# Performance work log

Measured on AMD Instinct MI355X. Metric: run time of the kernel, lower is better.

## Reference

```python
import jax, jax.numpy as jnp
import numpy as np

B, N, C_IN, HID, K, DEG = 8192, 64, 128, 128, 5, 8


def setup_inputs() -> dict:
    key = jax.random.key(0)
    ks = jax.random.split(key, 8)
    total = B * N
    E = B * N * DEG
    x = jax.random.normal(ks[0], (total, C_IN), dtype=jnp.float32)
    batch = jnp.repeat(jnp.arange(B, dtype=jnp.int64), N)
    g = jnp.repeat(jnp.arange(B, dtype=jnp.int64), N * DEG)
    src = g * N + jax.random.randint(ks[1], (E,), 0, N).astype(jnp.int64)
    dst = g * N + jax.random.randint(ks[2], (E,), 0, N).astype(jnp.int64)
    edge_index = jnp.stack([src, dst])  # [2, E]
    s = 0.05
    return {
        "x": x,
        "edge_index": edge_index,
        "batch": batch,
        "W_pool": jax.random.normal(ks[3], (C_IN, K), dtype=jnp.float32) * s,
        "b_pool": jnp.zeros((K,), jnp.float32),
        "W1": jax.random.normal(ks[4], (C_IN, HID), dtype=jnp.float32) * s,
        "b1": jnp.zeros((HID,), jnp.float32),
        "W2": jax.random.normal(ks[5], (HID, HID), dtype=jnp.float32) * s,
        "b2": jnp.zeros((HID,), jnp.float32),
        "W_lin": jax.random.normal(ks[6], (HID, 1), dtype=jnp.float32) * s,
        "b_lin": jnp.zeros((1,), jnp.float32),
        "num_graphs": B,
        "max_nodes": N,
    }


def dense_gcn(x, adj, W, b, mask=None):
    # PyG DenseGCNConv with add_loop=True: diagonal set to 1 on a copy
    n = adj.shape[1]
    idx = jnp.arange(n)
    adj_l = adj.at[:, idx, idx].set(1.0)
    out = x @ W  # [B, n, out]
    d = jnp.clip(adj_l.sum(-1), 1.0) ** -0.5  # [B, n]
    adj_n = d[:, :, None] * adj_l * d[:, None, :]
    out = jnp.einsum('bnm,bmc->bnc', adj_n, out) + b
    if mask is not None:
        out = out * mask[..., None]
    return out


def reference(x, edge_index, batch, W_pool, b_pool, W1, b1, W2, b2, W_lin, b_lin,
              num_graphs, max_nodes):
    total = x.shape[0]
    # to_dense_batch: position of each node within its graph (batch is sorted)
    first_idx = jax.ops.segment_min(jnp.arange(total), batch, num_segments=num_graphs)
    pos = jnp.arange(total) - first_idx[batch]
    x_dense = jnp.zeros((num_graphs, max_nodes, x.shape[1]), x.dtype).at[batch, pos].set(x)
    mask = jnp.zeros((num_graphs, max_nodes), x.dtype).at[batch, pos].set(1.0)
    # to_dense_adj
    src, dst = edge_index[0], edge_index[1]
    adj = jnp.zeros((num_graphs, max_nodes, max_nodes), x.dtype)
    adj = adj.at[batch[src], pos[src], pos[dst]].add(1.0)

    s = dense_gcn(x_dense, adj, W_pool, b_pool, mask)       # [B, N, K]
    x_l1 = dense_gcn(x_dense, adj, W1, b1, mask)            # [B, N, H]

    # dense_diff_pool (losses are discarded by the original forward)
    s = jax.nn.softmax(s, axis=-1) * mask[..., None]
    xm = x_l1 * mask[..., None]
    x_p1 = jnp.einsum('bnk,bnc->bkc', s, xm)                # [B, K, H]
    adj_p1 = jnp.einsum('bnk,bnm,bml->bkl', s, adj, s)      # [B, K, K]

    x_l2 = dense_gcn(x_p1, adj_p1, W2, b2)                  # [B, K, H]
    pooled = x_l2.sum(axis=1)                               # global_add_pool -> [B, H]
    return pooled @ W_lin + b_lin                           # [B, 1]
```

## Files before the change

### kernel.cpp

```cpp
#include <hip/hip_runtime.h>
#include <hip/hip_bf16.h>

#define NN 64
#define CI 128
#define HD 128
#define KC 5
#define SXS 136
#define AJW 17

#define WS_Z   9216
#define WS_B1Z 9344
#define WS_B2W 9345

typedef float v4f __attribute__((ext_vector_type(4)));
typedef __bf16 v8bf __attribute__((ext_vector_type(8)));
typedef unsigned short us8 __attribute__((ext_vector_type(8)));

__device__ __forceinline__ float us2f(unsigned short u) {
    union { unsigned i; float f; } v; v.i = ((unsigned)u) << 16; return v.f;
}
__device__ __forceinline__ unsigned short f2us(float f) {
    __hip_bfloat16 h = __float2bfloat16(f);
    return *reinterpret_cast<unsigned short*>(&h);
}

extern "C" __global__ void zprep(const float* __restrict__ W1,
                                 const float* __restrict__ Wp,
                                 const float* __restrict__ W2,
                                 const float* __restrict__ Wl,
                                 const float* __restrict__ b1,
                                 const float* __restrict__ b2,
                                 float* __restrict__ ws)
{
    const int b = blockIdx.x, t = threadIdx.x;
    if (b < 36) {
        const int ct = b >> 2, ks = b & 3;
        const int q = t >> 4, m16 = t & 15;
        const int k0 = ks * 32 + q * 8;
        us8 pk;
        #pragma unroll
        for (int j = 0; j < 8; ++j) {
            const int k = k0 + j;
            float v;
            if (ct < 8)      v = W1[k * HD + ct * 16 + m16];
            else             v = (m16 < KC) ? Wp[k * KC + m16] : 0.f;
            pk[j] = f2us(v);
        }
        reinterpret_cast<us8*>(ws)[b * 64 + t] = pk;
    } else if (b == 36) {
        float a0 = 0.f, a1 = 0.f;
        for (int c = 0; c < HD; ++c) {
            const float wl = Wl[c];
            a0 += W2[t * HD + c] * wl;
            a1 += W2[(t + 64) * HD + c] * wl;
        }
        ws[WS_Z + t] = a0;
        ws[WS_Z + 64 + t] = a1;
        float p1 = b1[t] * a0 + b1[t + 64] * a1;
        float p2 = b2[t] * Wl[t] + b2[t + 64] * Wl[t + 64];
        #pragma unroll
        for (int off = 32; off; off >>= 1) {
            p1 += __shfl_down(p1, off, 64);
            p2 += __shfl_down(p2, off, 64);
        }
        if (t == 0) { ws[WS_B1Z] = p1; ws[WS_B2W] = p2; }
    }
}

extern "C" __global__ __launch_bounds__(256, 5)
void diffpool_main(const float* __restrict__ x,
                   const int* __restrict__ ei,
                   const float* __restrict__ bp,
                   const float* __restrict__ bl,
                   const float* __restrict__ ws,
                   float* __restrict__ out,
                   int E, int epg)
{
    __shared__ __attribute__((aligned(16))) unsigned short sx[NN][SXS];
    __shared__ unsigned int sadjb[NN][AJW];
    __shared__ float sSm[NN][KC];
    __shared__ float spart[4][NN * KC];
    __shared__ float sz [HD];
    __shared__ float sqp[2][NN];
    __shared__ float sd [NN];
    __shared__ float sw_[NN];
    __shared__ unsigned int srdeg[NN];
    __shared__ float spp[4][25];
    __shared__ float sadjp[25];
    __shared__ float sd2[KC];
    __shared__ float scoef[KC + 1];

    const int t = threadIdx.x;
    const int g = blockIdx.x;
    const int lane = t & 63;
    const int wv = t >> 6;
    const int n = lane;
    const int h = wv;

    int e0s = -1, e0d = 0, e1s = -1, e1d = 0;
    const int base = g * epg;
    if (t < epg)       { e0s = ei[base + t] & 63;        e0d = ei[E + base + t] & 63; }
    if (t + 256 < epg) { e1s = ei[base + t + 256] & 63;  e1d = ei[E + base + t + 256] & 63; }

    {
        unsigned int* ap = &sadjb[0][0];
        for (int i = t; i < NN * AJW; i += 256) ap[i] = 0u;
        if (t < NN) srdeg[t] = 0u;
        const float* xg = x + (size_t)g * (NN * CI);
        #pragma unroll
        for (int i = 0; i < 4; ++i) {
            const int idx = t + 256 * i;
            const int row = idx >> 4, ch = idx & 15;
            const float4 v0 = *reinterpret_cast<const float4*>(xg + row * CI + ch * 8);
            const float4 v1 = *reinterpret_cast<const float4*>(xg + row * CI + ch * 8 + 4);
            us8 pk;
            pk[0] = f2us(v0.x); pk[1] = f2us(v0.y); pk[2] = f2us(v0.z); pk[3] = f2us(v0.w);
            pk[4] = f2us(v1.x); pk[5] = f2us(v1.y); pk[6] = f2us(v1.z); pk[7] = f2us(v1.w);
            *reinterpret_cast<us8*>(&sx[row][ch * 8]) = pk;
        }
        if (t < 32)
            reinterpret_cast<float4*>(sz)[t] = reinterpret_cast<const float4*>(ws + WS_Z)[t];
    }
    __syncthreads();

    {
        if (e0s >= 0) {
            atomicAdd(&sadjb[e0s][e0d >> 2], 1u << ((e0d & 3) * 8));
            atomicAdd(&srdeg[e0s], 1u);
        }
        if (e1s >= 0) {
            atomicAdd(&sadjb[e1s][e1d >> 2], 1u << ((e1d & 3) * 8));
            atomicAdd(&srdeg[e1s], 1u);
        }
        for (int j = t + 512; j < epg; j += 256) {
            const int sn = ei[base + j] & 63;
            const int dn = ei[E + base + j] & 63;
            atomicAdd(&sadjb[sn][dn >> 2], 1u << ((dn & 3) * 8));
            atomicAdd(&srdeg[sn], 1u);
        }
    }
    __syncthreads();

    {
        const int m16 = lane & 15;
        const int q = lane >> 4;
        const int arow = wv * 16 + m16;
        v8bf afrag[4];
        #pragma unroll
        for (int ks = 0; ks < 4; ++ks)
            afrag[ks] = *reinterpret_cast<const v8bf*>(&sx[arow][ks * 32 + q * 8]);
        const v8bf* wpk = reinterpret_cast<const v8bf*>(ws);
        #pragma unroll
        for (int ct = 0; ct < 9; ++ct) {
            v4f acc = {0.f, 0.f, 0.f, 0.f};
            #pragma unroll
            for (int ks = 0; ks < 4; ++ks) {
                const v8bf bfrag = wpk[(ct * 4 + ks) * 64 + lane];
                acc = __builtin_amdgcn_mfma_f32_16x16x32_bf16(afrag[ks], bfrag, acc, 0, 0, 0);
            }
            if (ct < 8) {
                #pragma unroll
                for (int r = 0; r < 4; ++r)
                    sx[wv * 16 + q * 4 + r][ct * 16 + m16] = f2us(acc[r]);
            } else if (m16 < KC) {
                #pragma unroll
                for (int r = 0; r < 4; ++r)
                    sSm[wv * 16 + q * 4 + r][m16] = acc[r];
            }
        }
    }
    if (t < NN) {
        const unsigned self = (sadjb[t][t >> 2] >> ((t & 3) * 8)) & 255u;
        sd[t] = rsqrtf((float)(srdeg[t] + 1u - self));
    }
    __syncthreads();

    {
        float a0 = 0.f, a1 = 0.f, a2 = 0.f, a3 = 0.f, a4 = 0.f;
        #pragma unroll
        for (int i = 0; i < 4; ++i) {
            const unsigned w = sadjb[n][h * 4 + i];
            #pragma unroll
            for (int b = 0; b < 4; ++b) {
                const int m = h * 16 + i * 4 + b;
                const float al = (m == n) ? 1.f : (float)((w >> (b * 8)) & 255u);
                const float f = al * sd[m];
                a0 += f * sSm[m][0]; a1 += f * sSm[m][1]; a2 += f * sSm[m][2];
                a3 += f * sSm[m][3]; a4 += f * sSm[m][4];
            }
        }
        float* pp = &spart[h][n * KC];
        pp[0] = a0; pp[1] = a1; pp[2] = a2; pp[3] = a3; pp[4] = a4;
    }
    __syncthreads();

    if (wv == 0) {
        float a0 = spart[0][n*KC+0] + spart[1][n*KC+0] + spart[2][n*KC+0] + spart[3][n*KC+0];
        float a1 = spart[0][n*KC+1] + spart[1][n*KC+1] + spart[2][n*KC+1] + spart[3][n*KC+1];
        float a2 = spart[0][n*KC+2] + spart[1][n*KC+2] + spart[2][n*KC+2] + spart[3][n*KC+2];
        float a3 = spart[0][n*KC+3] + spart[1][n*KC+3] + spart[2][n*KC+3] + spart[3][n*KC+3];
        float a4 = spart[0][n*KC+4] + spart[1][n*KC+4] + spart[2][n*KC+4] + spart[3][n*KC+4];
        const float dn = sd[n];
        a0 = a0 * dn + bp[0]; a1 = a1 * dn + bp[1]; a2 = a2 * dn + bp[2];
        a3 = a3 * dn + bp[3]; a4 = a4 * dn + bp[4];
        const float mx = fmaxf(fmaxf(fmaxf(a0, a1), fmaxf(a2, a3)), a4);
        a0 = expf(a0 - mx); a1 = expf(a1 - mx); a2 = expf(a2 - mx);
        a3 = expf(a3 - mx); a4 = expf(a4 - mx);
        const float inv = 1.f / (a0 + a1 + a2 + a3 + a4);
        sSm[n][0] = a0 * inv; sSm[n][1] = a1 * inv; sSm[n][2] = a2 * inv;
        sSm[n][3] = a3 * inv; sSm[n][4] = a4 * inv;
    } else if (wv <= 2) {
        const int p = wv - 1, m = lane;
        float a = 0.f;
        #pragma unroll
        for (int cc = 0; cc < 8; ++cc) {
            const int c = (cc + (m >> 3)) & 7;
            const us8 hh = *reinterpret_cast<const us8*>(&sx[m][p * 64 + c * 8]);
            #pragma unroll
            for (int j = 0; j < 8; ++j) a += us2f(hh[j]) * sz[p * 64 + c * 8 + j];
        }
        sqp[p][m] = a;
    }
    __syncthreads();

    {
        float u0 = 0.f, u1 = 0.f, u2 = 0.f, u3 = 0.f, u4 = 0.f;
        #pragma unroll
        for (int i = 0; i < 4; ++i) {
            const unsigned w = sadjb[n][h * 4 + i];
            #pragma unroll
            for (int b = 0; b < 4; ++b) {
                const int m = h * 16 + i * 4 + b;
                const float c = (float)((w >> (b * 8)) & 255u);
                u0 += c * sSm[m][0]; u1 += c * sSm[m][1]; u2 += c * sSm[m][2];
                u3 += c * sSm[m][3]; u4 += c * sSm[m][4];
            }
        }
        float* pp = &spart[h][n * KC];
        pp[0] = u0; pp[1] = u1; pp[2] = u2; pp[3] = u3; pp[4] = u4;
    }
    __syncthreads();

    if (lane < 25) {
        const int k = lane / 5, l = lane - k * 5;
        float a = 0.f;
        #pragma unroll
        for (int i = 0; i < 16; ++i) {
            const int m = h * 16 + i;
            const float u = spart[0][m*KC+l] + spart[1][m*KC+l] +
                            spart[2][m*KC+l] + spart[3][m*KC+l];
            a += sSm[m][k] * u;
        }
        spp[h][lane] = a;
    }
    __syncthreads();

    if (wv == 0) {
        if (lane < 25)
            sadjp[lane] = spp[0][lane] + spp[1][lane] + spp[2][lane] + spp[3][lane];
        if (lane < KC) {
            float s_ = 0.f;
            #pragma unroll
            for (int l = 0; l < KC; ++l) s_ += sadjp[lane * KC + l];
            s_ += 1.f - sadjp[lane * 6];
            sd2[lane] = rsqrtf(fmaxf(s_, 1.f));
        }
        if (lane < KC) {
            float a = 0.f;
            #pragma unroll
            for (int k = 0; k < KC; ++k) a += sd2[k] * sadjp[k * KC + lane];
            a += sd2[lane] * (1.f - sadjp[lane * 6]);
            scoef[lane] = sd2[lane] * a;
        }
        float t5 = scoef[0] * sSm[n][0] + scoef[1] * sSm[n][1] + scoef[2] * sSm[n][2] +
                   scoef[3] * sSm[n][3] + scoef[4] * sSm[n][4];
        sw_[n] = sd[n] * t5;
        #pragma unroll
        for (int off = 32; off; off >>= 1) t5 += __shfl_down(t5, off, 64);
        if (lane == 0) scoef[KC] = t5;
    }
    __syncthreads();

    {
        float pa = 0.f;
        #pragma unroll
        for (int i = 0; i < 16; ++i) {
            const int nn2 = h * 16 + i;
            const float al = (nn2 == n) ? 1.f
                           : (float)((sadjb[nn2][n >> 2] >> ((n & 3) * 8)) & 255u);
            pa += sw_[nn2] * al;
        }
        spart[h][n] = pa;
    }
    __syncthreads();

    if (wv == 0) {
        const float a = spart[0][n] + spart[1][n] + spart[2][n] + spart[3][n];
        const float qm = sqp[0][n] + sqp[1][n];
        float v = sd[n] * a * qm;
        #pragma unroll
        for (int off = 32; off; off >>= 1) v += __shfl_down(v, off, 64);
        if (lane == 0)
            out[g] = v + scoef[KC] * ws[WS_B1Z] + 5.f * ws[WS_B2W] + bl[0];
    }
}

extern "C" void kernel_launch(void* const* d_in, const int* in_sizes, int n_in,
                              void* d_out, int out_size, void* d_ws, size_t ws_size,
                              hipStream_t stream) {
    const float* x  = (const float*)d_in[0];
    const int*   ei = (const int*)d_in[1];
    const float* Wp = (const float*)d_in[3];
    const float* bp = (const float*)d_in[4];
    const float* W1 = (const float*)d_in[5];
    const float* b1 = (const float*)d_in[6];
    const float* W2 = (const float*)d_in[7];
    const float* b2 = (const float*)d_in[8];
    const float* Wl = (const float*)d_in[9];
    const float* bl = (const float*)d_in[10];
    float* out = (float*)d_out;
    float* ws  = (float*)d_ws;

    const int B = out_size;
    const int E = in_sizes[1] / 2;
    const int epg = E / B;

    zprep<<<37, 64, 0, stream>>>(W1, Wp, W2, Wl, b1, b2, ws);
    diffpool_main<<<B, 256, 0, stream>>>(x, ei, bp, bl, ws, out, E, epg);
}
```

Measured before the change: 474.1 us.

## Fold W1 into precomputed vector y and drop per-graph W1 MFMA

Precomputes y = W1·(W2·Wl) once in the prep kernel, so each graph only needs a dot product x·y per node, computed during the x load with shuffle reductions. This removes the eight 16-column W1 MFMA tiles and the bf16 hidden-state round trip through shared memory. The change also overlaps several shared buffers in a union, keeps per-lane values in registers to remove a few barriers, and raises the occupancy hint to 6. The q path now uses fp32 x instead of bf16-rounded hidden features, which changes numerics slightly.

After: 423.6 us. -10.6%, faster.

```diff
diff --git a/kernel.cpp b/kernel.cpp
--- a/kernel.cpp
+++ b/kernel.cpp
@@ -8,17 +8,14 @@
 #define SXS 136
 #define AJW 17
 
-#define WS_Z   9216
-#define WS_B1Z 9344
-#define WS_B2W 9345
+#define WS_Y   1024
+#define WS_B1Z 1152
+#define WS_B2W 1153
 
 typedef float v4f __attribute__((ext_vector_type(4)));
 typedef __bf16 v8bf __attribute__((ext_vector_type(8)));
 typedef unsigned short us8 __attribute__((ext_vector_type(8)));
 
-__device__ __forceinline__ float us2f(unsigned short u) {
-    union { unsigned i; float f; } v; v.i = ((unsigned)u) << 16; return v.f;
-}
 __device__ __forceinline__ unsigned short f2us(float f) {
     __hip_bfloat16 h = __float2bfloat16(f);
     return *reinterpret_cast<unsigned short*>(&h);
@@ -33,29 +30,26 @@
                                  float* __restrict__ ws)
 {
     const int b = blockIdx.x, t = threadIdx.x;
-    if (b < 36) {
-        const int ct = b >> 2, ks = b & 3;
+    if (b < 4) {
+        const int ks = b;
         const int q = t >> 4, m16 = t & 15;
         const int k0 = ks * 32 + q * 8;
         us8 pk;
         #pragma unroll
         for (int j = 0; j < 8; ++j) {
             const int k = k0 + j;
-            float v;
-            if (ct < 8)      v = W1[k * HD + ct * 16 + m16];
-            else             v = (m16 < KC) ? Wp[k * KC + m16] : 0.f;
-            pk[j] = f2us(v);
+            pk[j] = f2us((m16 < KC) ? Wp[k * KC + m16] : 0.f);
         }
         reinterpret_cast<us8*>(ws)[b * 64 + t] = pk;
-    } else if (b == 36) {
+    } else {
+        __shared__ float sz_[HD];
         float a0 = 0.f, a1 = 0.f;
         for (int c = 0; c < HD; ++c) {
             const float wl = Wl[c];
             a0 += W2[t * HD + c] * wl;
             a1 += W2[(t + 64) * HD + c] * wl;
         }
-        ws[WS_Z + t] = a0;
-        ws[WS_Z + 64 + t] = a1;
+        sz_[t] = a0; sz_[t + 64] = a1;
         float p1 = b1[t] * a0 + b1[t + 64] * a1;
         float p2 = b2[t] * Wl[t] + b2[t + 64] * Wl[t + 64];
         #pragma unroll
@@ -64,10 +58,18 @@
             p2 += __shfl_down(p2, off, 64);
         }
         if (t == 0) { ws[WS_B1Z] = p1; ws[WS_B2W] = p2; }
+        __syncthreads();
+        #pragma unroll
+        for (int rr = 0; rr < 2; ++rr) {
+            const int r = t + rr * 64;
+            float acc = 0.f;
+            for (int h2 = 0; h2 < HD; ++h2) acc += W1[r * HD + h2] * sz_[h2];
+            ws[WS_Y + r] = acc;
+        }
     }
 }
 
-extern "C" __global__ __launch_bounds__(256, 5)
+extern "C" __global__ __launch_bounds__(256, 6)
 void diffpool_main(const float* __restrict__ x,
                    const int* __restrict__ ei,
                    const float* __restrict__ bp,
@@ -76,19 +78,23 @@
                    float* __restrict__ out,
                    int E, int epg)
 {
-    __shared__ __attribute__((aligned(16))) unsigned short sx[NN][SXS];
+    __shared__ __attribute__((aligned(16))) union {
+        unsigned short sx[NN][SXS];
+        struct {
+            float A[4][NN * KC];
+            float Bu[4][NN * KC];
+            float pp[4][25];
+        } s;
+    } u;
     __shared__ unsigned int sadjb[NN][AJW];
     __shared__ float sSm[NN][KC];
-    __shared__ float spart[4][NN * KC];
-    __shared__ float sz [HD];
-    __shared__ float sqp[2][NN];
-    __shared__ float sd [NN];
+    __shared__ float sq[NN];
+    __shared__ float sd[NN];
     __shared__ float sw_[NN];
     __shared__ unsigned int srdeg[NN];
-    __shared__ float spp[4][25];
     __shared__ float sadjp[25];
     __shared__ float sd2[KC];
-    __shared__ float scoef[KC + 1];
+    __shared__ float scoef[KC];
 
     const int t = threadIdx.x;
     const int g = blockIdx.x;
@@ -97,6 +103,13 @@
     const int n = lane;
     const int h = wv;
 
+    const float bp0 = bp[0], bp1 = bp[1], bp2 = bp[2], bp3 = bp[3], bp4 = bp[4];
+    const float c_b1z = ws[WS_B1Z], c_b2w = ws[WS_B2W], c_bl = bl[0];
+
+    const int ch = t & 15;
+    const float4 y0 = *reinterpret_cast<const float4*>(ws + WS_Y + ch * 8);
+    const float4 y1 = *reinterpret_cast<const float4*>(ws + WS_Y + ch * 8 + 4);
+
     int e0s = -1, e0d = 0, e1s = -1, e1d = 0;
     const int base = g * epg;
     if (t < epg)       { e0s = ei[base + t] & 63;        e0d = ei[E + base + t] & 63; }
@@ -109,17 +122,21 @@
         const float* xg = x + (size_t)g * (NN * CI);
         #pragma unroll
         for (int i = 0; i < 4; ++i) {
-            const int idx = t + 256 * i;
-            const int row = idx >> 4, ch = idx & 15;
+            const int row = (t >> 4) + 16 * i;
             const float4 v0 = *reinterpret_cast<const float4*>(xg + row * CI + ch * 8);
             const float4 v1 = *reinterpret_cast<const float4*>(xg + row * CI + ch * 8 + 4);
             us8 pk;
             pk[0] = f2us(v0.x); pk[1] = f2us(v0.y); pk[2] = f2us(v0.z); pk[3] = f2us(v0.w);
             pk[4] = f2us(v1.x); pk[5] = f2us(v1.y); pk[6] = f2us(v1.z); pk[7] = f2us(v1.w);
-            *reinterpret_cast<us8*>(&sx[row][ch * 8]) = pk;
-        }
-        if (t < 32)
-            reinterpret_cast<float4*>(sz)[t] = reinterpret_cast<const float4*>(ws + WS_Z)[t];
+            *reinterpret_cast<us8*>(&u.sx[row][ch * 8]) = pk;
+            float qp = v0.x * y0.x + v0.y * y0.y + v0.z * y0.z + v0.w * y0.w
+                     + v1.x * y1.x + v1.y * y1.y + v1.z * y1.z + v1.w * y1.w;
+            qp += __shfl_down(qp, 8, 16);
+            qp += __shfl_down(qp, 4, 16);
+            qp += __shfl_down(qp, 2, 16);
+            qp += __shfl_down(qp, 1, 16);
+            if (ch == 0) sq[row] = qp;
+        }
     }
     __syncthreads();
 
@@ -139,104 +156,82 @@
             atomicAdd(&srdeg[sn], 1u);
         }
     }
-    __syncthreads();
-
     {
         const int m16 = lane & 15;
         const int q = lane >> 4;
         const int arow = wv * 16 + m16;
-        v8bf afrag[4];
-        #pragma unroll
-        for (int ks = 0; ks < 4; ++ks)
-            afrag[ks] = *reinterpret_cast<const v8bf*>(&sx[arow][ks * 32 + q * 8]);
         const v8bf* wpk = reinterpret_cast<const v8bf*>(ws);
-        #pragma unroll
-        for (int ct = 0; ct < 9; ++ct) {
-            v4f acc = {0.f, 0.f, 0.f, 0.f};
-            #pragma unroll
-            for (int ks = 0; ks < 4; ++ks) {
-                const v8bf bfrag = wpk[(ct * 4 + ks) * 64 + lane];
-                acc = __builtin_amdgcn_mfma_f32_16x16x32_bf16(afrag[ks], bfrag, acc, 0, 0, 0);
-            }
-            if (ct < 8) {
-                #pragma unroll
-                for (int r = 0; r < 4; ++r)
-                    sx[wv * 16 + q * 4 + r][ct * 16 + m16] = f2us(acc[r]);
-            } else if (m16 < KC) {
-                #pragma unroll
-                for (int r = 0; r < 4; ++r)
-                    sSm[wv * 16 + q * 4 + r][m16] = acc[r];
-            }
-        }
-    }
-    if (t < NN) {
-        const unsigned self = (sadjb[t][t >> 2] >> ((t & 3) * 8)) & 255u;
-        sd[t] = rsqrtf((float)(srdeg[t] + 1u - self));
-    }
-    __syncthreads();
-
-    {
+        v4f acc = {0.f, 0.f, 0.f, 0.f};
+        #pragma unroll
+        for (int ks = 0; ks < 4; ++ks) {
+            const v8bf afrag = *reinterpret_cast<const v8bf*>(&u.sx[arow][ks * 32 + q * 8]);
+            acc = __builtin_amdgcn_mfma_f32_16x16x32_bf16(afrag, wpk[ks * 64 + lane], acc, 0, 0, 0);
+        }
+        if (m16 < KC) {
+            #pragma unroll
+            for (int r = 0; r < 4; ++r)
+                sSm[wv * 16 + q * 4 + r][m16] = acc[r];
+        }
+    }
+    __syncthreads();
+
+    unsigned aw0, aw1, aw2, aw3;
+    float dlane;
+    {
+        const unsigned selfb = (sadjb[lane][lane >> 2] >> ((lane & 3) * 8)) & 255u;
+        dlane = rsqrtf((float)(srdeg[lane] + 1u - selfb));
+        sd[lane] = dlane;
+        aw0 = sadjb[n][h * 4 + 0];
+        aw1 = sadjb[n][h * 4 + 1];
+        aw2 = sadjb[n][h * 4 + 2];
+        aw3 = sadjb[n][h * 4 + 3];
         float a0 = 0.f, a1 = 0.f, a2 = 0.f, a3 = 0.f, a4 = 0.f;
         #pragma unroll
         for (int i = 0; i < 4; ++i) {
-            const unsigned w = sadjb[n][h * 4 + i];
-            #pragma unroll
-            for (int b = 0; b < 4; ++b) {
-                const int m = h * 16 + i * 4 + b;
-                const float al = (m == n) ? 1.f : (float)((w >> (b * 8)) & 255u);
+            const unsigned w = (i == 0) ? aw0 : (i == 1) ? aw1 : (i == 2) ? aw2 : aw3;
+            #pragma unroll
+            for (int bb = 0; bb < 4; ++bb) {
+                const int m = h * 16 + i * 4 + bb;
+                const float al = (m == n) ? 1.f : (float)((w >> (bb * 8)) & 255u);
                 const float f = al * sd[m];
                 a0 += f * sSm[m][0]; a1 += f * sSm[m][1]; a2 += f * sSm[m][2];
                 a3 += f * sSm[m][3]; a4 += f * sSm[m][4];
             }
         }
-        float* pp = &spart[h][n * KC];
+        float* pp = &u.s.A[h][n * KC];
         pp[0] = a0; pp[1] = a1; pp[2] = a2; pp[3] = a3; pp[4] = a4;
     }
     __syncthreads();
 
-    if (wv == 0) {
-        float a0 = spart[0][n*KC+0] + spart[1][n*KC+0] + spart[2][n*KC+0] + spart[3][n*KC+0];
-        float a1 = spart[0][n*KC+1] + spart[1][n*KC+1] + spart[2][n*KC+1] + spart[3][n*KC+1];
-        float a2 = spart[0][n*KC+2] + spart[1][n*KC+2] + spart[2][n*KC+2] + spart[3][n*KC+2];
-        float a3 = spart[0][n*KC+3] + spart[1][n*KC+3] + spart[2][n*KC+3] + spart[3][n*KC+3];
-        float a4 = spart[0][n*KC+4] + spart[1][n*KC+4] + spart[2][n*KC+4] + spart[3][n*KC+4];
-        const float dn = sd[n];
-        a0 = a0 * dn + bp[0]; a1 = a1 * dn + bp[1]; a2 = a2 * dn + bp[2];
-        a3 = a3 * dn + bp[3]; a4 = a4 * dn + bp[4];
+    float s0v, s1v, s2v, s3v, s4v;
+    {
+        float a0 = u.s.A[0][n*KC+0] + u.s.A[1][n*KC+0] + u.s.A[2][n*KC+0] + u.s.A[3][n*KC+0];
+        float a1 = u.s.A[0][n*KC+1] + u.s.A[1][n*KC+1] + u.s.A[2][n*KC+1] + u.s.A[3][n*KC+1];
+        float a2 = u.s.A[0][n*KC+2] + u.s.A[1][n*KC+2] + u.s.A[2][n*KC+2] + u.s.A[3][n*KC+2];
+        float a3 = u.s.A[0][n*KC+3] + u.s.A[1][n*KC+3] + u.s.A[2][n*KC+3] + u.s.A[3][n*KC+3];
+        float a4 = u.s.A[0][n*KC+4] + u.s.A[1][n*KC+4] + u.s.A[2][n*KC+4] + u.s.A[3][n*KC+4];
+        a0 = a0 * dlane + bp0; a1 = a1 * dlane + bp1; a2 = a2 * dlane + bp2;
+        a3 = a3 * dlane + bp3; a4 = a4 * dlane + bp4;
         const float mx = fmaxf(fmaxf(fmaxf(a0, a1), fmaxf(a2, a3)), a4);
         a0 = expf(a0 - mx); a1 = expf(a1 - mx); a2 = expf(a2 - mx);
         a3 = expf(a3 - mx); a4 = expf(a4 - mx);
         const float inv = 1.f / (a0 + a1 + a2 + a3 + a4);
-        sSm[n][0] = a0 * inv; sSm[n][1] = a1 * inv; sSm[n][2] = a2 * inv;
-        sSm[n][3] = a3 * inv; sSm[n][4] = a4 * inv;
-    } else if (wv <= 2) {
-        const int p = wv - 1, m = lane;
-        float a = 0.f;
-        #pragma unroll
-        for (int cc = 0; cc < 8; ++cc) {
-            const int c = (cc + (m >> 3)) & 7;
-            const us8 hh = *reinterpret_cast<const us8*>(&sx[m][p * 64 + c * 8]);
-            #pragma unroll
-            for (int j = 0; j < 8; ++j) a += us2f(hh[j]) * sz[p * 64 + c * 8 + j];
-        }
-        sqp[p][m] = a;
-    }
-    __syncthreads();
-
-    {
+        s0v = a0 * inv; s1v = a1 * inv; s2v = a2 * inv; s3v = a3 * inv; s4v = a4 * inv;
+        sSm[n][0] = s0v; sSm[n][1] = s1v; sSm[n][2] = s2v;
+        sSm[n][3] = s3v; sSm[n][4] = s4v;
         float u0 = 0.f, u1 = 0.f, u2 = 0.f, u3 = 0.f, u4 = 0.f;
         #pragma unroll
         for (int i = 0; i < 4; ++i) {
-            const unsigned w = sadjb[n][h * 4 + i];
-            #pragma unroll
-            for (int b = 0; b < 4; ++b) {
-                const int m = h * 16 + i * 4 + b;
-                const float c = (float)((w >> (b * 8)) & 255u);
+            const unsigned w = (i == 0) ? aw0 : (i == 1) ? aw1 : (i == 2) ? aw2 : aw3;
+            #pragma unroll
+            for (int bb = 0; bb < 4; ++bb) {
+                const int m = h * 16 + i * 4 + bb;
+                const float c = (float)((w >> (bb * 8)) & 255u);
                 u0 += c * sSm[m][0]; u1 += c * sSm[m][1]; u2 += c * sSm[m][2];
                 u3 += c * sSm[m][3]; u4 += c * sSm[m][4];
             }
         }
-        float* pp = &spart[h][n * KC];
+        float* pp = &u.s.Bu[h][n * KC];
         pp[0] = u0; pp[1] = u1; pp[2] = u2; pp[3] = u3; pp[4] = u4;
     }
     __syncthreads();
@@ -247,17 +242,18 @@
         #pragma unroll
         for (int i = 0; i < 16; ++i) {
             const int m = h * 16 + i;
-            const float u = spart[0][m*KC+l] + spart[1][m*KC+l] +
-                            spart[2][m*KC+l] + spart[3][m*KC+l];
-            a += sSm[m][k] * u;
-        }
-        spp[h][lane] = a;
-    }
-    __syncthreads();
-
-    if (wv == 0) {
+            const float uu = u.s.Bu[0][m*KC+l] + u.s.Bu[1][m*KC+l]
+                           + u.s.Bu[2][m*KC+l] + u.s.Bu[3][m*KC+l];
+            a += sSm[m][k] * uu;
+        }
+        u.s.pp[h][lane] = a;
+    }
+    __syncthreads();
+
+    float cbv;
+    {
         if (lane < 25)
-            sadjp[lane] = spp[0][lane] + spp[1][lane] + spp[2][lane] + spp[3][lane];
+            sadjp[lane] = u.s.pp[0][lane] + u.s.pp[1][lane] + u.s.pp[2][lane] + u.s.pp[3][lane];
         if (lane < KC) {
             float s_ = 0.f;
             #pragma unroll
@@ -272,16 +268,12 @@
             a += sd2[lane] * (1.f - sadjp[lane * 6]);
             scoef[lane] = sd2[lane] * a;
         }
-        float t5 = scoef[0] * sSm[n][0] + scoef[1] * sSm[n][1] + scoef[2] * sSm[n][2] +
-                   scoef[3] * sSm[n][3] + scoef[4] * sSm[n][4];
-        sw_[n] = sd[n] * t5;
-        #pragma unroll
-        for (int off = 32; off; off >>= 1) t5 += __shfl_down(t5, off, 64);
-        if (lane == 0) scoef[KC] = t5;
-    }
-    __syncthreads();
-
-    {
+        float t5 = scoef[0] * s0v + scoef[1] * s1v + scoef[2] * s2v +
+                   scoef[3] * s3v + scoef[4] * s4v;
+        sw_[n] = dlane * t5;
+        cbv = t5;
+        #pragma unroll
+        for (int off = 32; off; off >>= 1) cbv += __shfl_down(cbv, off, 64);
         float pa = 0.f;
         #pragma unroll
         for (int i = 0; i < 16; ++i) {
@@ -290,18 +282,17 @@
                            : (float)((sadjb[nn2][n >> 2] >> ((n & 3) * 8)) & 255u);
             pa += sw_[nn2] * al;
         }
-        spart[h][n] = pa;
+        u.s.A[h][n] = pa;
     }
     __syncthreads();
 
     if (wv == 0) {
-        const float a = spart[0][n] + spart[1][n] + spart[2][n] + spart[3][n];
-        const float qm = sqp[0][n] + sqp[1][n];
-        float v = sd[n] * a * qm;
+        const float a = u.s.A[0][n] + u.s.A[1][n] + u.s.A[2][n] + u.s.A[3][n];
+        float v = dlane * a * sq[n];
         #pragma unroll
         for (int off = 32; off; off >>= 1) v += __shfl_down(v, off, 64);
         if (lane == 0)
-            out[g] = v + scoef[KC] * ws[WS_B1Z] + 5.f * ws[WS_B2W] + bl[0];
+            out[g] = v + cbv * c_b1z + 5.f * c_b2w + c_bl;
     }
 }
 
@@ -325,6 +316,6 @@
     const int E = in_sizes[1] / 2;
     const int epg = E / B;
 
-    zprep<<<37, 64, 0, stream>>>(W1, Wp, W2, Wl, b1, b2, ws);
+    zprep<<<5, 64, 0, stream>>>(W1, Wp, W2, Wl, b1, b2, ws);
     diffpool_main<<<B, 256, 0, stream>>>(x, ei, bp, bl, ws, out, E, epg);
 }
```
